# Performance work log

Measured on AMD Instinct MI355X. Metric: run time of the kernel, lower is better.

Reference implementation:

```python
import jax, jax.numpy as jnp
import numpy as np

B, T, D = 8, 2048, 1024


def setup_inputs() -> dict:
    key = jax.random.key(0)
    ks = jax.random.split(key, 9)
    s = 1.0 / np.sqrt(D)
    return {
        "e": jax.random.normal(ks[0], (B, T, D), jnp.float32),
        "residual": jax.random.normal(ks[1], (B, T, D), jnp.float32),
        "Wq_w": jax.random.normal(ks[2], (D, D), jnp.float32) * s,
        "Wq_b": jax.random.normal(ks[3], (D,), jnp.float32) * s,
        "Wk_w": jax.random.normal(ks[4], (D, D), jnp.float32) * s,
        "Wk_b": jax.random.normal(ks[5], (D,), jnp.float32) * s,
        "Wv_w": jax.random.normal(ks[6], (D, D), jnp.float32) * s,
        "Wv_b": jax.random.normal(ks[7], (D,), jnp.float32) * s,
        "v_table": jax.random.normal(ks[8], (T, 1), jnp.float32),
    }


def reference(e, residual, Wq_w, Wq_b, Wk_w, Wk_b, Wv_w, Wv_b, v_table):
    T_ = e.shape[1]
    # relative position index: pos[i,j] = max(i - j, 0)
    pos = jnp.arange(T_)
    rel = jnp.maximum(pos[:, None] - pos[None, :], 0)          # (T, T) int
    pos_embd = v_table[rel, 0]                                 # (T, T) gather from Embedding(length, 1)

    # torch Linear: x @ W.T + b
    Q = e @ Wq_w.T + Wq_b                                      # (B, T, D)
    K = residual @ Wk_w.T + Wk_b                               # (B, T, D)
    V = e @ Wv_w.T + Wv_b                                      # (B, T, D)

    # Q @ K^T  (torch: Q @ Wk(residual).transpose(-2,-1))
    scores = jnp.einsum('btd,bsd->bts', Q, K)                  # (B, T, T)
    # einsum('BeT,Tt->BTt', K^T, pos_embd) == sum_e K[B,T,e] * pos_embd[T,t]
    scores = scores + K.sum(-1)[:, :, None] * pos_embd[None]   # (B, T, T)

    # causal mask via tril (zeros strictly-upper entries); NO softmax in this variant
    scores = scores * jnp.tril(jnp.ones((T_, T_), scores.dtype))
    return scores @ V                                          # (B, T, D)
```

## Files before the change

kernel.cpp:

```cpp
#include <hip/hip_runtime.h>

typedef unsigned short u16;
typedef __attribute__((ext_vector_type(8))) short bf16x8;
typedef __attribute__((ext_vector_type(8))) unsigned short u16x8;
typedef __attribute__((ext_vector_type(4))) float f32x4;

#define AS1 __attribute__((address_space(1)))
#define AS3 __attribute__((address_space(3)))

static __device__ __forceinline__ u16 f2bf(float f) {
  unsigned u = __float_as_uint(f);
  u += 0x7FFFu + ((u >> 16) & 1u);
  return (u16)(u >> 16);
}

__global__ __launch_bounds__(256) void conv_all(
    const float* __restrict__ e, const float* __restrict__ res,
    const float* __restrict__ wq, const float* __restrict__ wk,
    const float* __restrict__ wv,
    u16* __restrict__ eb, u16* __restrict__ rb,
    u16* __restrict__ oq, u16* __restrict__ ok, u16* __restrict__ ov,
    float* __restrict__ ksum) {
  const int z = blockIdx.z;
  if (z < 2) {
    int i = blockIdx.x * 256 + threadIdx.x;
    const float* in = z ? res : e;
    u16* out = z ? rb : eb;
    const float4* p = (const float4*)in + (size_t)i * 2;
    float4 a = p[0], b = p[1];
    u16x8 r;
    r[0] = f2bf(a.x); r[1] = f2bf(a.y); r[2] = f2bf(a.z); r[3] = f2bf(a.w);
    r[4] = f2bf(b.x); r[5] = f2bf(b.y); r[6] = f2bf(b.z); r[7] = f2bf(b.w);
    ((u16x8*)out)[i] = r;
    return;
  }
  const int bx = blockIdx.x;
  if (bx < 1536) {
    const int sel = bx >> 9;
    const int i = (bx & 511) * 256 + threadIdx.x;
    const float* in = sel == 0 ? wq : (sel == 1 ? wk : wv);
    u16* out = sel == 0 ? oq : (sel == 1 ? ok : ov);
    const float4* p = (const float4*)in + (size_t)i * 2;
    float4 a = p[0], b = p[1];
    u16x8 r;
    r[0] = f2bf(a.x); r[1] = f2bf(a.y); r[2] = f2bf(a.z); r[3] = f2bf(a.w);
    r[4] = f2bf(b.x); r[5] = f2bf(b.y); r[6] = f2bf(b.z); r[7] = f2bf(b.w);
    ((u16x8*)out)[i] = r;
  } else if (bx < 1544) {
    const int i = (bx - 1536) * 256 + threadIdx.x;
#pragma unroll
    for (int j = 0; j < 8; ++j) ksum[i * 8 + j] = 0.f;
  }
}

enum { M_BIASN = 0, M_BIASM = 1, M_SCORES = 2, M_OUT = 3 };

template <int MODE>
static __device__ __forceinline__ void core128(
    const u16* __restrict__ Ab, int lda, const u16* __restrict__ Bb, int ldb,
    char* smem, int m0, int n0, int nk, void* __restrict__ Cbase, int ldc,
    const float* __restrict__ bias, const float* __restrict__ ksb,
    const float* __restrict__ vtab, float* __restrict__ ksum_acc) {
  const int tid = threadIdx.x;
  const int lane = tid & 63;
  const int wid = tid >> 6;
  const int wm = wid >> 1, wn = wid & 1;

  char* As = smem;
  char* Bs = smem + 16384;

  const int rbase_st = tid >> 3;
  const int gcol = ((tid & 7) << 4) ^ ((rbase_st & 7) << 4);

  const int aoff = (wm * 64 + (lane & 15)) * 128;
  const int boff = (wn * 64 + (lane & 15)) * 128;
  const int c0 = ((0 * 4 + (lane >> 4)) ^ (lane & 7)) << 4;
  const int c1 = ((1 * 4 + (lane >> 4)) ^ (lane & 7)) << 4;

  f32x4 acc[4][4];
#pragma unroll
  for (int m = 0; m < 4; ++m)
#pragma unroll
    for (int n = 0; n < 4; ++n) acc[m][n] = (f32x4){0.f, 0.f, 0.f, 0.f};

  for (int kt = 0; kt < nk; ++kt) {
    const int k0 = kt * 64;
#pragma unroll
    for (int i = 0; i < 4; ++i) {
      const char* ga = (const char*)(Ab + (size_t)(m0 + i * 32 + rbase_st) * lda + k0) + gcol;
      __builtin_amdgcn_global_load_lds(
          (const AS1 void*)ga, (AS3 void*)(As + i * 4096 + wid * 1024), 16, 0, 0);
    }
#pragma unroll
    for (int i = 0; i < 4; ++i) {
      const char* gb = (const char*)(Bb + (size_t)(n0 + i * 32 + rbase_st) * ldb + k0) + gcol;
      __builtin_amdgcn_global_load_lds(
          (const AS1 void*)gb, (AS3 void*)(Bs + i * 4096 + wid * 1024), 16, 0, 0);
    }
    __syncthreads();
#pragma unroll
    for (int ks = 0; ks < 2; ++ks) {
      const int cks = ks ? c1 : c0;
      bf16x8 af[4], bfv[4];
#pragma unroll
      for (int m = 0; m < 4; ++m) af[m] = *(const bf16x8*)(As + aoff + m * 2048 + cks);
#pragma unroll
      for (int n = 0; n < 4; ++n) bfv[n] = *(const bf16x8*)(Bs + boff + n * 2048 + cks);
#pragma unroll
      for (int m = 0; m < 4; ++m)
#pragma unroll
        for (int n = 0; n < 4; ++n)
          acc[m][n] = __builtin_amdgcn_mfma_f32_16x16x32_bf16(af[m], bfv[n], acc[m][n], 0, 0, 0);
    }
    __syncthreads();
  }

  u16* C16 = (u16*)Cbase;
  float* Cf = (float*)Cbase;
  float rs[4][4];
  if (MODE == M_BIASN && ksum_acc) {
#pragma unroll
    for (int m = 0; m < 4; ++m)
#pragma unroll
      for (int j = 0; j < 4; ++j) rs[m][j] = 0.f;
  }
#pragma unroll
  for (int m = 0; m < 4; ++m) {
#pragma unroll
    for (int n = 0; n < 4; ++n) {
      const int rb = m0 + wm * 64 + m * 16 + ((lane >> 4) << 2);
      const int c = n0 + wn * 64 + n * 16 + (lane & 15);
#pragma unroll
      for (int j = 0; j < 4; ++j) {
        const int r = rb + j;
        float v = acc[m][n][j];
        if (MODE == M_BIASN) {
          v += bias[c];
          if (ksum_acc) rs[m][j] += v;
          C16[(size_t)r * ldc + c] = f2bf(v);
        } else if (MODE == M_BIASM) {
          v += bias[r];
          C16[(size_t)r * ldc + c] = f2bf(v);
        } else if (MODE == M_SCORES) {
          if (c <= r) v += ksb[r] * vtab[r - c];
          else v = 0.f;
          C16[(size_t)r * ldc + c] = f2bf(v);
        } else {
          Cf[(size_t)r * ldc + c] = v;
        }
      }
    }
  }
  if (MODE == M_BIASN && ksum_acc) {
#pragma unroll
    for (int m = 0; m < 4; ++m) {
      const int rb = m0 + wm * 64 + m * 16 + ((lane >> 4) << 2);
#pragma unroll
      for (int j = 0; j < 4; ++j) {
        float s = rs[m][j];
        s += __shfl_xor(s, 1);
        s += __shfl_xor(s, 2);
        s += __shfl_xor(s, 4);
        s += __shfl_xor(s, 8);
        if ((lane & 15) == 0) atomicAdd(&ksum_acc[rb + j], s);
      }
    }
  }
}

__global__ __launch_bounds__(256, 4) void k_qkv_proj(
    const u16* eb, const u16* rb, const u16* Wq, const u16* Wk, const u16* Wv,
    const float* bq, const float* bk, const float* bv,
    u16* Q, u16* K, u16* VT, float* ksum) {
  const int l = blockIdx.x;
  const int xcd = l & 7;
  const int idx = l >> 3;
  const int j = idx & 127;
  __shared__ char smem[32768];
  if (idx < 256) {
    const bool isK = idx >= 128;
    const int gy = xcd * 16 + (j >> 3);
    const int gx = j & 7;
    core128<M_BIASN>(isK ? rb : eb, 1024, isK ? Wk : Wq, 1024, smem,
                     gy * 128, gx * 128, 16, isK ? K : Q, 1024,
                     isK ? bk : bq, nullptr, nullptr, isK ? ksum : nullptr);
  } else {
    const int gxt = xcd * 16 + (j >> 3);
    const int gyd = j & 7;
    core128<M_BIASM>(Wv, 1024, eb, 1024, smem, gyd * 128, gxt * 128, 16,
                     VT, 16384, bv, nullptr, nullptr, nullptr);
  }
}
__global__ __launch_bounds__(256, 4) void k_scores(
    const u16* Q, const u16* K, u16* S, const float* ksum, const float* vtab) {
  const int l = blockIdx.x;
  const int z = l & 7;
  const int h = l >> 3;
  int gy = 0;
#pragma unroll
  for (int q = 1; q < 16; ++q) if (q * (q + 1) / 2 <= h) gy = q;
  const int gx = h - gy * (gy + 1) / 2;
  __shared__ char smem[32768];
  core128<M_SCORES>(Q + (size_t)z * 2048 * 1024, 1024,
                    K + (size_t)z * 2048 * 1024, 1024, smem,
                    gy * 128, gx * 128, 16,
                    S + (size_t)z * 2048 * 2048, 2048,
                    nullptr, ksum + (size_t)z * 2048, vtab, nullptr);
}
__global__ __launch_bounds__(256, 4) void k_out(
    const u16* S, const u16* VT, float* O) {
  const int l = blockIdx.x;
  const int z = l & 7;
  const int idx = l >> 3;
  const int r = idx >> 5;
  const int p = idx & 31;
  const int rank = (r << 5) | ((r & 1) ? (31 - p) : p);
  const int gy = 15 - (rank >> 3);
  const int gx = rank & 7;
  const int nk = (gy + 1) * 2;
  __shared__ char smem[32768];
  core128<M_OUT>(S + (size_t)z * 2048 * 2048, 2048,
                 VT + (size_t)z * 2048, 16384, smem,
                 gy * 128, gx * 128, nk,
                 O + (size_t)z * 2048 * 1024, 1024,
                 nullptr, nullptr, nullptr, nullptr);
}

extern "C" void kernel_launch(void* const* d_in, const int* in_sizes, int n_in,
                              void* d_out, int out_size, void* d_ws, size_t ws_size,
                              hipStream_t stream) {
  (void)in_sizes; (void)n_in; (void)out_size; (void)ws_size;
  const float* e    = (const float*)d_in[0];
  const float* res  = (const float*)d_in[1];
  const float* Wq_w = (const float*)d_in[2];
  const float* Wq_b = (const float*)d_in[3];
  const float* Wk_w = (const float*)d_in[4];
  const float* Wk_b = (const float*)d_in[5];
  const float* Wv_w = (const float*)d_in[6];
  const float* Wv_b = (const float*)d_in[7];
  const float* vtab = (const float*)d_in[8];

  char* ws = (char*)d_ws;
  const size_t SZ = 33554432;
  u16* ebf = (u16*)(ws);
  u16* rbf = (u16*)(ws + SZ);
  u16* Qb  = (u16*)(ws + 2 * SZ);
  u16* Kb  = (u16*)(ws + 3 * SZ);
  u16* VT  = (u16*)(ws + 4 * SZ);
  u16* Wqb = (u16*)(ws + 5 * SZ);
  u16* Wkb = (u16*)(ws + 5 * SZ + 2097152);
  u16* Wvb = (u16*)(ws + 5 * SZ + 2 * 2097152);
  float* ksum = (float*)(ws + 5 * SZ + 3 * 2097152);
  u16* scores = (u16*)(ws);

  conv_all<<<dim3(8192, 1, 3), 256, 0, stream>>>(e, res, Wq_w, Wk_w, Wv_w,
                                                 ebf, rbf, Wqb, Wkb, Wvb, ksum);

  k_qkv_proj<<<dim3(3072, 1, 1), 256, 0, stream>>>(ebf, rbf, Wqb, Wkb, Wvb,
                                                   Wq_b, Wk_b, Wv_b, Qb, Kb, VT, ksum);

  k_scores<<<dim3(1088, 1, 1), 256, 0, stream>>>(Qb, Kb, scores, ksum, vtab);

  k_out<<<dim3(1024, 1, 1), 256, 0, stream>>>(scores, VT, (float*)d_out);
}
```

Before: 248.6 us.

## Fuse fp32-to-bf16 activation conversion into QKV projection GEMM loads

Drops the separate pass that converted e and residual to bf16 in workspace, and instead loads fp32 activation tiles directly inside the projection GEMM. They are converted with packed bf16 instructions and written swizzled into shared memory. This removes a full write and re-read of the converted activations. In exchange, the GEMM reads twice the bytes per activation tile through registers rather than direct global-to-LDS loads, which raises register pressure.

```diff
diff --git a/kernel.cpp b/kernel.cpp
--- a/kernel.cpp
+++ b/kernel.cpp
@@ -4,6 +4,7 @@
 typedef __attribute__((ext_vector_type(8))) short bf16x8;
 typedef __attribute__((ext_vector_type(8))) unsigned short u16x8;
 typedef __attribute__((ext_vector_type(4))) float f32x4;
+typedef __attribute__((ext_vector_type(4))) unsigned int u32x4;
 
 #define AS1 __attribute__((address_space(1)))
 #define AS3 __attribute__((address_space(3)))
@@ -14,26 +15,11 @@
   return (u16)(u >> 16);
 }
 
-__global__ __launch_bounds__(256) void conv_all(
-    const float* __restrict__ e, const float* __restrict__ res,
+__global__ __launch_bounds__(256) void conv_w2(
     const float* __restrict__ wq, const float* __restrict__ wk,
     const float* __restrict__ wv,
-    u16* __restrict__ eb, u16* __restrict__ rb,
     u16* __restrict__ oq, u16* __restrict__ ok, u16* __restrict__ ov,
     float* __restrict__ ksum) {
-  const int z = blockIdx.z;
-  if (z < 2) {
-    int i = blockIdx.x * 256 + threadIdx.x;
-    const float* in = z ? res : e;
-    u16* out = z ? rb : eb;
-    const float4* p = (const float4*)in + (size_t)i * 2;
-    float4 a = p[0], b = p[1];
-    u16x8 r;
-    r[0] = f2bf(a.x); r[1] = f2bf(a.y); r[2] = f2bf(a.z); r[3] = f2bf(a.w);
-    r[4] = f2bf(b.x); r[5] = f2bf(b.y); r[6] = f2bf(b.z); r[7] = f2bf(b.w);
-    ((u16x8*)out)[i] = r;
-    return;
-  }
   const int bx = blockIdx.x;
   if (bx < 1536) {
     const int sel = bx >> 9;
@@ -46,7 +32,7 @@
     r[0] = f2bf(a.x); r[1] = f2bf(a.y); r[2] = f2bf(a.z); r[3] = f2bf(a.w);
     r[4] = f2bf(b.x); r[5] = f2bf(b.y); r[6] = f2bf(b.z); r[7] = f2bf(b.w);
     ((u16x8*)out)[i] = r;
-  } else if (bx < 1544) {
+  } else {
     const int i = (bx - 1536) * 256 + threadIdx.x;
 #pragma unroll
     for (int j = 0; j < 8; ++j) ksum[i * 8 + j] = 0.f;
@@ -55,9 +41,10 @@
 
 enum { M_BIASN = 0, M_BIASM = 1, M_SCORES = 2, M_OUT = 3 };
 
-template <int MODE>
+template <int MODE, int F32A, int F32B>
 static __device__ __forceinline__ void core128(
-    const u16* __restrict__ Ab, int lda, const u16* __restrict__ Bb, int ldb,
+    const u16* __restrict__ Ab, const float* __restrict__ Af, int lda,
+    const u16* __restrict__ Bb, const float* __restrict__ Bf, int ldb,
     char* smem, int m0, int n0, int nk, void* __restrict__ Cbase, int ldc,
     const float* __restrict__ bias, const float* __restrict__ ksb,
     const float* __restrict__ vtab, float* __restrict__ ksum_acc) {
@@ -72,6 +59,11 @@
   const int rbase_st = tid >> 3;
   const int gcol = ((tid & 7) << 4) ^ ((rbase_st & 7) << 4);
 
+  const int srow = tid >> 1;
+  const int shalf = (tid & 1) * 32;
+  char* sdstA = As + srow * 128;
+  char* sdstB = Bs + srow * 128;
+
   const int aoff = (wm * 64 + (lane & 15)) * 128;
   const int boff = (wn * 64 + (lane & 15)) * 128;
   const int c0 = ((0 * 4 + (lane >> 4)) ^ (lane & 7)) << 4;
@@ -85,17 +77,60 @@
 
   for (int kt = 0; kt < nk; ++kt) {
     const int k0 = kt * 64;
-#pragma unroll
-    for (int i = 0; i < 4; ++i) {
-      const char* ga = (const char*)(Ab + (size_t)(m0 + i * 32 + rbase_st) * lda + k0) + gcol;
-      __builtin_amdgcn_global_load_lds(
-          (const AS1 void*)ga, (AS3 void*)(As + i * 4096 + wid * 1024), 16, 0, 0);
-    }
-#pragma unroll
-    for (int i = 0; i < 4; ++i) {
-      const char* gb = (const char*)(Bb + (size_t)(n0 + i * 32 + rbase_st) * ldb + k0) + gcol;
-      __builtin_amdgcn_global_load_lds(
-          (const AS1 void*)gb, (AS3 void*)(Bs + i * 4096 + wid * 1024), 16, 0, 0);
+    float4 va[8], vb[8];
+    if (F32A) {
+      const float4* ga = (const float4*)(Af + (size_t)(m0 + srow) * lda + k0 + shalf);
+#pragma unroll
+      for (int i = 0; i < 8; ++i) va[i] = ga[i];
+    }
+    if (F32B) {
+      const float4* gb = (const float4*)(Bf + (size_t)(n0 + srow) * ldb + k0 + shalf);
+#pragma unroll
+      for (int i = 0; i < 8; ++i) vb[i] = gb[i];
+    }
+    if (!F32A) {
+#pragma unroll
+      for (int i = 0; i < 4; ++i) {
+        const char* ga = (const char*)(Ab + (size_t)(m0 + i * 32 + rbase_st) * lda + k0) + gcol;
+        __builtin_amdgcn_global_load_lds(
+            (const AS1 void*)ga, (AS3 void*)(As + i * 4096 + wid * 1024), 16, 0, 0);
+      }
+    }
+    if (!F32B) {
+#pragma unroll
+      for (int i = 0; i < 4; ++i) {
+        const char* gb = (const char*)(Bb + (size_t)(n0 + i * 32 + rbase_st) * ldb + k0) + gcol;
+        __builtin_amdgcn_global_load_lds(
+            (const AS1 void*)gb, (AS3 void*)(Bs + i * 4096 + wid * 1024), 16, 0, 0);
+      }
+    }
+    if (F32A) {
+      unsigned w[16];
+#pragma unroll
+      for (int i = 0; i < 8; ++i) {
+        asm("v_cvt_pk_bf16_f32 %0, %1, %2" : "=v"(w[2 * i]) : "v"(va[i].x), "v"(va[i].y));
+        asm("v_cvt_pk_bf16_f32 %0, %1, %2" : "=v"(w[2 * i + 1]) : "v"(va[i].z), "v"(va[i].w));
+      }
+#pragma unroll
+      for (int u = 0; u < 4; ++u) {
+        const int c = shalf * 2 + u * 16;
+        *(u32x4*)(sdstA + (c ^ ((srow & 7) << 4))) =
+            (u32x4){w[4 * u], w[4 * u + 1], w[4 * u + 2], w[4 * u + 3]};
+      }
+    }
+    if (F32B) {
+      unsigned w[16];
+#pragma unroll
+      for (int i = 0; i < 8; ++i) {
+        asm("v_cvt_pk_bf16_f32 %0, %1, %2" : "=v"(w[2 * i]) : "v"(vb[i].x), "v"(vb[i].y));
+        asm("v_cvt_pk_bf16_f32 %0, %1, %2" : "=v"(w[2 * i + 1]) : "v"(vb[i].z), "v"(vb[i].w));
+      }
+#pragma unroll
+      for (int u = 0; u < 4; ++u) {
+        const int c = shalf * 2 + u * 16;
+        *(u32x4*)(sdstB + (c ^ ((srow & 7) << 4))) =
+            (u32x4){w[4 * u], w[4 * u + 1], w[4 * u + 2], w[4 * u + 3]};
+      }
     }
     __syncthreads();
 #pragma unroll
@@ -169,7 +204,7 @@
 }
 
 __global__ __launch_bounds__(256, 4) void k_qkv_proj(
-    const u16* eb, const u16* rb, const u16* Wq, const u16* Wk, const u16* Wv,
+    const float* e, const float* res, const u16* Wq, const u16* Wk, const u16* Wv,
     const float* bq, const float* bk, const float* bv,
     u16* Q, u16* K, u16* VT, float* ksum) {
   const int l = blockIdx.x;
@@ -181,14 +216,16 @@
     const bool isK = idx >= 128;
     const int gy = xcd * 16 + (j >> 3);
     const int gx = j & 7;
-    core128<M_BIASN>(isK ? rb : eb, 1024, isK ? Wk : Wq, 1024, smem,
-                     gy * 128, gx * 128, 16, isK ? K : Q, 1024,
-                     isK ? bk : bq, nullptr, nullptr, isK ? ksum : nullptr);
+    core128<M_BIASN, 1, 0>(nullptr, isK ? res : e, 1024,
+                           isK ? Wk : Wq, nullptr, 1024, smem,
+                           gy * 128, gx * 128, 16, isK ? K : Q, 1024,
+                           isK ? bk : bq, nullptr, nullptr, isK ? ksum : nullptr);
   } else {
     const int gxt = xcd * 16 + (j >> 3);
     const int gyd = j & 7;
-    core128<M_BIASM>(Wv, 1024, eb, 1024, smem, gyd * 128, gxt * 128, 16,
-                     VT, 16384, bv, nullptr, nullptr, nullptr);
+    core128<M_BIASM, 0, 1>(Wv, nullptr, 1024, nullptr, e, 1024, smem,
+                           gyd * 128, gxt * 128, 16,
+                           VT, 16384, bv, nullptr, nullptr, nullptr);
   }
 }
 __global__ __launch_bounds__(256, 4) void k_scores(
@@ -201,11 +238,11 @@
   for (int q = 1; q < 16; ++q) if (q * (q + 1) / 2 <= h) gy = q;
   const int gx = h - gy * (gy + 1) / 2;
   __shared__ char smem[32768];
-  core128<M_SCORES>(Q + (size_t)z * 2048 * 1024, 1024,
-                    K + (size_t)z * 2048 * 1024, 1024, smem,
-                    gy * 128, gx * 128, 16,
-                    S + (size_t)z * 2048 * 2048, 2048,
-                    nullptr, ksum + (size_t)z * 2048, vtab, nullptr);
+  core128<M_SCORES, 0, 0>(Q + (size_t)z * 2048 * 1024, nullptr, 1024,
+                          K + (size_t)z * 2048 * 1024, nullptr, 1024, smem,
+                          gy * 128, gx * 128, 16,
+                          S + (size_t)z * 2048 * 2048, 2048,
+                          nullptr, ksum + (size_t)z * 2048, vtab, nullptr);
 }
 __global__ __launch_bounds__(256, 4) void k_out(
     const u16* S, const u16* VT, float* O) {
@@ -219,11 +256,11 @@
   const int gx = rank & 7;
   const int nk = (gy + 1) * 2;
   __shared__ char smem[32768];
-  core128<M_OUT>(S + (size_t)z * 2048 * 2048, 2048,
-                 VT + (size_t)z * 2048, 16384, smem,
-                 gy * 128, gx * 128, nk,
-                 O + (size_t)z * 2048 * 1024, 1024,
-                 nullptr, nullptr, nullptr, nullptr);
+  core128<M_OUT, 0, 0>(S + (size_t)z * 2048 * 2048, nullptr, 2048,
+                       VT + (size_t)z * 2048, nullptr, 16384, smem,
+                       gy * 128, gx * 128, nk,
+                       O + (size_t)z * 2048 * 1024, 1024,
+                       nullptr, nullptr, nullptr, nullptr);
 }
 
 extern "C" void kernel_launch(void* const* d_in, const int* in_sizes, int n_in,
@@ -242,8 +279,7 @@
 
   char* ws = (char*)d_ws;
   const size_t SZ = 33554432;
-  u16* ebf = (u16*)(ws);
-  u16* rbf = (u16*)(ws + SZ);
+  u16* scores = (u16*)(ws);
   u16* Qb  = (u16*)(ws + 2 * SZ);
   u16* Kb  = (u16*)(ws + 3 * SZ);
   u16* VT  = (u16*)(ws + 4 * SZ);
@@ -251,12 +287,10 @@
   u16* Wkb = (u16*)(ws + 5 * SZ + 2097152);
   u16* Wvb = (u16*)(ws + 5 * SZ + 2 * 2097152);
   float* ksum = (float*)(ws + 5 * SZ + 3 * 2097152);
-  u16* scores = (u16*)(ws);
-
-  conv_all<<<dim3(8192, 1, 3), 256, 0, stream>>>(e, res, Wq_w, Wk_w, Wv_w,
-                                                 ebf, rbf, Wqb, Wkb, Wvb, ksum);
-
-  k_qkv_proj<<<dim3(3072, 1, 1), 256, 0, stream>>>(ebf, rbf, Wqb, Wkb, Wvb,
+
+  conv_w2<<<dim3(1544, 1, 1), 256, 0, stream>>>(Wq_w, Wk_w, Wv_w, Wqb, Wkb, Wvb, ksum);
+
+  k_qkv_proj<<<dim3(3072, 1, 1), 256, 0, stream>>>(e, res, Wqb, Wkb, Wvb,
                                                    Wq_b, Wk_b, Wv_b, Qb, Kb, VT, ksum);
 
   k_scores<<<dim3(1088, 1, 1), 256, 0, stream>>>(Qb, Kb, scores, ksum, vtab);
```

New measurement: 383.5 us. 1.54x slower.

## Rewrite causal scores GEMM with 256x128 tiles and 512-thread blocks

Applied to the files above, without the earlier changes.

Replaces the generic 128x128 core routine for the Q·K^T scores kernel with a dedicated kernel. Each block computes a 256x128 tile using 8 waves and direct global-to-LDS loads into swizzled shared memory. The epilogue fuses the relative-position term (ksum·vtab) and the causal mask, then writes bf16 scores. Taller tiles increase reuse of the K operand and cut the block count. The trade-offs are extra wasted work on diagonal tiles, single-buffered loads with no overlap, and scalar per-element stores in the epilogue.

```diff
diff --git a/kernel.cpp b/kernel.cpp
--- a/kernel.cpp
+++ b/kernel.cpp
@@ -191,22 +191,95 @@
                      VT, 16384, bv, nullptr, nullptr, nullptr);
   }
 }
-__global__ __launch_bounds__(256, 4) void k_scores(
+
+__global__ __launch_bounds__(512, 4) void k_scores(
     const u16* Q, const u16* K, u16* S, const float* ksum, const float* vtab) {
   const int l = blockIdx.x;
   const int z = l & 7;
-  const int h = l >> 3;
+  const int idx = l >> 3;
   int gy = 0;
 #pragma unroll
-  for (int q = 1; q < 16; ++q) if (q * (q + 1) / 2 <= h) gy = q;
-  const int gx = h - gy * (gy + 1) / 2;
-  __shared__ char smem[32768];
-  core128<M_SCORES>(Q + (size_t)z * 2048 * 1024, 1024,
-                    K + (size_t)z * 2048 * 1024, 1024, smem,
-                    gy * 128, gx * 128, 16,
-                    S + (size_t)z * 2048 * 2048, 2048,
-                    nullptr, ksum + (size_t)z * 2048, vtab, nullptr);
-}
+  for (int q = 1; q < 8; ++q) if (q * q + q <= idx) gy = q;
+  const int gx = idx - (gy * gy + gy);
+  const u16* Qb = Q + (size_t)z * 2048 * 1024;
+  const u16* Kb = K + (size_t)z * 2048 * 1024;
+  u16* Sb = S + (size_t)z * 2048 * 2048;
+  const float* ksb = ksum + (size_t)z * 2048;
+  const int m0 = gy * 256, n0 = gx * 128;
+
+  __shared__ char smem[49152];
+  char* As = smem;
+  char* Bs = smem + 32768;
+
+  const int tid = threadIdx.x;
+  const int lane = tid & 63;
+  const int wid = tid >> 6;
+  const int wm = wid >> 1, wn = wid & 1;
+
+  const int strow = tid >> 3;
+  const int gcol = ((tid & 7) << 4) ^ ((strow & 7) << 4);
+
+  const int aoff = (wm * 64 + (lane & 15)) * 128;
+  const int boff = (wn * 64 + (lane & 15)) * 128;
+  const int c0 = (((lane >> 4)) ^ (lane & 7)) << 4;
+  const int c1 = ((4 + (lane >> 4)) ^ (lane & 7)) << 4;
+
+  f32x4 acc[4][4];
+#pragma unroll
+  for (int m = 0; m < 4; ++m)
+#pragma unroll
+    for (int n = 0; n < 4; ++n) acc[m][n] = (f32x4){0.f, 0.f, 0.f, 0.f};
+
+  for (int kt = 0; kt < 16; ++kt) {
+    const int k0 = kt * 64;
+#pragma unroll
+    for (int i = 0; i < 4; ++i) {
+      const char* ga = (const char*)(Qb + (size_t)(m0 + i * 64 + strow) * 1024 + k0) + gcol;
+      __builtin_amdgcn_global_load_lds(
+          (const AS1 void*)ga, (AS3 void*)(As + i * 8192 + wid * 1024), 16, 0, 0);
+    }
+#pragma unroll
+    for (int i = 0; i < 2; ++i) {
+      const char* gb = (const char*)(Kb + (size_t)(n0 + i * 64 + strow) * 1024 + k0) + gcol;
+      __builtin_amdgcn_global_load_lds(
+          (const AS1 void*)gb, (AS3 void*)(Bs + i * 8192 + wid * 1024), 16, 0, 0);
+    }
+    __syncthreads();
+#pragma unroll
+    for (int ks = 0; ks < 2; ++ks) {
+      const int cks = ks ? c1 : c0;
+      bf16x8 af[4], bfv[4];
+#pragma unroll
+      for (int m = 0; m < 4; ++m) af[m] = *(const bf16x8*)(As + aoff + m * 2048 + cks);
+#pragma unroll
+      for (int n = 0; n < 4; ++n) bfv[n] = *(const bf16x8*)(Bs + boff + n * 2048 + cks);
+#pragma unroll
+      for (int m = 0; m < 4; ++m)
+#pragma unroll
+        for (int n = 0; n < 4; ++n)
+          acc[m][n] = __builtin_amdgcn_mfma_f32_16x16x32_bf16(af[m], bfv[n], acc[m][n], 0, 0, 0);
+    }
+    __syncthreads();
+  }
+
+#pragma unroll
+  for (int m = 0; m < 4; ++m) {
+#pragma unroll
+    for (int n = 0; n < 4; ++n) {
+      const int rb = m0 + wm * 64 + m * 16 + ((lane >> 4) << 2);
+      const int c = n0 + wn * 64 + n * 16 + (lane & 15);
+#pragma unroll
+      for (int j = 0; j < 4; ++j) {
+        const int r = rb + j;
+        float v = acc[m][n][j];
+        if (c <= r) v += ksb[r] * vtab[r - c];
+        else v = 0.f;
+        Sb[(size_t)r * 2048 + c] = f2bf(v);
+      }
+    }
+  }
+}
+
 __global__ __launch_bounds__(256, 4) void k_out(
     const u16* S, const u16* VT, float* O) {
   const int l = blockIdx.x;
@@ -259,7 +332,7 @@
   k_qkv_proj<<<dim3(3072, 1, 1), 256, 0, stream>>>(ebf, rbf, Wqb, Wkb, Wvb,
                                                    Wq_b, Wk_b, Wv_b, Qb, Kb, VT, ksum);
 
-  k_scores<<<dim3(1088, 1, 1), 256, 0, stream>>>(Qb, Kb, scores, ksum, vtab);
+  k_scores<<<dim3(576, 1, 1), 512, 0, stream>>>(Qb, Kb, scores, ksum, vtab);
 
   k_out<<<dim3(1024, 1, 1), 256, 0, stream>>>(scores, VT, (float*)d_out);
 }
```

New measurement: 255.6 us. 2.8% more time.
